# Kernel tuning notes

Measured on AMD Instinct MI355X. Metric: run time of the kernel, lower is better.

## Reference

```python
import jax, jax.numpy as jnp
import numpy as np

B, T, D_IN = 4, 512, 2048
H, G, HD = 16, 4, 128
CACHE = 3584
S = CACHE + T  # max_seq after cache concat
MAX_POS = 8192
EPS = 1e-6


def _rope_tables():
    inv_freq = 1.0 / (10000.0 ** (np.arange(0, HD, 2, dtype=np.float32) / HD))
    pos = np.arange(MAX_POS, dtype=np.float32)
    freqs = np.outer(pos, inv_freq)                      # [MAX_POS, HD//2]
    emb = np.concatenate([freqs, freqs], axis=-1)        # [MAX_POS, HD]
    return jnp.asarray(np.cos(emb)), jnp.asarray(np.sin(emb))


def setup_inputs() -> dict:
    key = jax.random.key(0)
    ks = jax.random.split(key, 8)
    cos, sin = _rope_tables()
    sc = 1.0 / float(np.sqrt(D_IN))
    x = jax.random.normal(ks[0], (B, T, D_IN), jnp.float32)
    mask = jnp.zeros((B, 1, T, S), bool)  # True = masked out
    position_ids = jnp.broadcast_to(CACHE + jnp.arange(T, dtype=jnp.int32), (B, T))
    cache_k = jax.random.normal(ks[1], (B, G, CACHE, HD), jnp.float32)
    cache_v = jax.random.normal(ks[2], (B, G, CACHE, HD), jnp.float32)
    q_w = jax.random.normal(ks[3], (D_IN, H * HD), jnp.float32) * sc
    k_w = jax.random.normal(ks[4], (D_IN, G * HD), jnp.float32) * sc
    v_w = jax.random.normal(ks[5], (D_IN, G * HD), jnp.float32) * sc
    o_w = jax.random.normal(ks[6], (H * HD, D_IN), jnp.float32) * sc
    qn_w = jnp.ones((HD,), jnp.float32)
    kn_w = jnp.ones((HD,), jnp.float32)
    return dict(x=x, mask=mask, cos=cos, sin=sin, position_ids=position_ids,
                cache_k=cache_k, cache_v=cache_v, q_w=q_w, k_w=k_w, v_w=v_w,
                o_w=o_w, qn_w=qn_w, kn_w=kn_w)


def _rms(z, w):
    return z * jax.lax.rsqrt(jnp.mean(z * z, axis=-1, keepdims=True) + EPS) * w


def _rot_half(z):
    z1, z2 = jnp.split(z, 2, axis=-1)
    return jnp.concatenate([-z2, z1], axis=-1)


def _rope(z, c, s):
    return z * c + _rot_half(z) * s


def reference(x, mask, cos, sin, position_ids, cache_k, cache_v,
              q_w, k_w, v_w, o_w, qn_w, kn_w):
    b, t, _ = x.shape
    # projections + per-head RMSNorm (norm over head_dim, order-independent of transpose)
    q = _rms((x @ q_w).reshape(b, t, H, HD), qn_w).transpose(0, 2, 1, 3)  # [b,H,t,hd]
    k = _rms((x @ k_w).reshape(b, t, G, HD), kn_w).transpose(0, 2, 1, 3)  # [b,G,t,hd]
    v = (x @ v_w).reshape(b, t, G, HD).transpose(0, 2, 1, 3)              # [b,G,t,hd]
    c = cos[position_ids][:, None]  # [b,1,t,hd]
    s = sin[position_ids][:, None]
    q = _rope(q, c, s)
    k = _rope(k, c, s)
    # KV-cache concat (uniform prev length == padded max_seq in the original)
    k_full = jnp.concatenate([cache_k, k], axis=2)  # [b,G,S,hd]
    v_full = jnp.concatenate([cache_v, v], axis=2)
    # GQA attention: group queries over KV heads
    qg = q.reshape(b, G, H // G, t, HD)
    scores = jnp.einsum('bghtd,bgsd->bghts', qg, k_full) * (1.0 / float(np.sqrt(HD)))
    scores = scores + jnp.where(mask[:, :, None], -jnp.inf, 0.0)  # mask [b,1,t,S]->[b,1,1,t,S]
    attn = jax.nn.softmax(scores, axis=-1)
    ctx = jnp.einsum('bghts,bgsd->bghtd', attn, v_full)
    ctx = ctx.reshape(b, H, t, HD).transpose(0, 2, 1, 3).reshape(b, t, H * HD)
    return (ctx @ o_w, k_full, v_full)
```

## Files before the change

kernel.cpp:

```cpp
#include <hip/hip_runtime.h>
#include <stdint.h>

typedef unsigned short u16;
typedef __attribute__((ext_vector_type(4))) float f32x4;
typedef __attribute__((ext_vector_type(8))) short s16x8;

__device__ inline u16 f2b(float f){
    uint32_t u = __builtin_bit_cast(uint32_t, f);
    uint32_t r = (u + 0x7fffu + ((u >> 16) & 1u)) >> 16;
    return (u16)r;
}
__device__ inline float b2f(u16 u){
    uint32_t x = ((uint32_t)u) << 16;
    return __builtin_bit_cast(float, x);
}

__global__ void convert_x_k(const float* __restrict__ src, u16* __restrict__ dst, int n4){
    int i = blockIdx.x * blockDim.x + threadIdx.x;
    if (i >= n4) return;
    float4 v = ((const float4*)src)[i];
    ushort4 o; o.x = f2b(v.x); o.y = f2b(v.y); o.z = f2b(v.z); o.w = f2b(v.w);
    ((ushort4*)dst)[i] = o;
}

__global__ void transpose_convert_k(const float* __restrict__ src, u16* __restrict__ dst,
                                    int srcCols, int dstLd, int rowOff){
    __shared__ float ls[64][68];
    int r0 = blockIdx.x * 64;
    int c0 = blockIdx.y * 64;
    int t = threadIdx.x;
    #pragma unroll
    for (int i = 0; i < 4; i++){
        int r = i * 16 + (t >> 4);
        int c = (t & 15) * 4;
        float4 v = *(const float4*)(src + (size_t)(r0 + r) * srcCols + c0 + c);
        *(float4*)&ls[r][c] = v;
    }
    __syncthreads();
    #pragma unroll
    for (int i = 0; i < 2; i++){
        int rr = i * 32 + (t >> 3);
        int cc = (t & 7) * 8;
        union { u16 u[8]; uint4 v; } o;
        #pragma unroll
        for (int j = 0; j < 8; j++) o.u[j] = f2b(ls[cc + j][rr]);
        *(uint4*)(dst + (size_t)(rowOff + c0 + rr) * dstLd + r0 + cc) = o.v;
    }
}

__global__ void copy_cache_k_k(const float* __restrict__ ck, float* __restrict__ kfull,
                               u16* __restrict__ kbf, int n4){
    int i = blockIdx.x * blockDim.x + threadIdx.x;
    if (i >= n4) return;
    const int per_bg = 3584 * 128 / 4;
    int bg = i / per_bg, rem = i - bg * per_bg;
    float4 v = ((const float4*)ck)[i];
    size_t dst4 = (size_t)bg * (4096 * 128 / 4) + rem;
    ((float4*)kfull)[dst4] = v;
    ushort4 o; o.x = f2b(v.x); o.y = f2b(v.y); o.z = f2b(v.z); o.w = f2b(v.w);
    ((ushort4*)kbf)[dst4] = o;
}

__global__ void transpose_cache_v_k(const float* __restrict__ cv, float* __restrict__ vfull,
                                    u16* __restrict__ vT){
    __shared__ float ls[64][68];
    int bg = blockIdx.z;
    int s0 = blockIdx.x * 64;
    int d0 = blockIdx.y * 64;
    int t = threadIdx.x;
    #pragma unroll
    for (int i = 0; i < 4; i++){
        int r = i * 16 + (t >> 4);
        int c = (t & 15) * 4;
        float4 v = *(const float4*)(cv + ((size_t)bg * 3584 + s0 + r) * 128 + d0 + c);
        *(float4*)&ls[r][c] = v;
        *(float4*)(vfull + ((size_t)bg * 4096 + s0 + r) * 128 + d0 + c) = v;
    }
    __syncthreads();
    #pragma unroll
    for (int i = 0; i < 2; i++){
        int rr = i * 32 + (t >> 3);
        int cc = (t & 7) * 8;
        union { u16 u[8]; uint4 v; } o;
        #pragma unroll
        for (int j = 0; j < 8; j++) o.u[j] = f2b(ls[cc + j][rr]);
        *(uint4*)(vT + ((size_t)bg * 128 + d0 + rr) * 4096 + s0 + cc) = o.v;
    }
}

__global__ __launch_bounds__(256) void gemm_bt_k(const u16* __restrict__ A, const u16* __restrict__ Bt,
                                                 float* __restrict__ C, int K, int N){
    __shared__ u16 As[128][72];
    __shared__ u16 Bs[128][72];
    int m0 = blockIdx.y * 128;
    int n0 = blockIdx.x * 128;
    int t = threadIdx.x;
    int wave = t >> 6, lane = t & 63;
    int g16 = lane >> 4, l16 = lane & 15;
    int wr = (wave >> 1) * 64, wc = (wave & 1) * 64;
    f32x4 acc[4][4] = {};
    for (int k0 = 0; k0 < K; k0 += 64){
        #pragma unroll
        for (int i = 0; i < 4; i++){
            int r = i * 32 + (t >> 3);
            int cg = (t & 7) * 8;
            *(uint4*)&As[r][cg] = *(const uint4*)(A + (size_t)(m0 + r) * K + k0 + cg);
            *(uint4*)&Bs[r][cg] = *(const uint4*)(Bt + (size_t)(n0 + r) * K + k0 + cg);
        }
        __syncthreads();
        #pragma unroll
        for (int kc = 0; kc < 2; kc++){
            s16x8 af[4], bfx[4];
            #pragma unroll
            for (int mi = 0; mi < 4; mi++) af[mi]  = *(const s16x8*)&As[wr + mi * 16 + l16][kc * 32 + g16 * 8];
            #pragma unroll
            for (int ni = 0; ni < 4; ni++) bfx[ni] = *(const s16x8*)&Bs[wc + ni * 16 + l16][kc * 32 + g16 * 8];
            #pragma unroll
            for (int mi = 0; mi < 4; mi++)
                #pragma unroll
                for (int ni = 0; ni < 4; ni++)
                    acc[mi][ni] = __builtin_amdgcn_mfma_f32_16x16x32_bf16(af[mi], bfx[ni], acc[mi][ni], 0, 0, 0);
        }
        __syncthreads();
    }
    #pragma unroll
    for (int mi = 0; mi < 4; mi++)
        #pragma unroll
        for (int ni = 0; ni < 4; ni++)
            #pragma unroll
            for (int r = 0; r < 4; r++){
                int row = m0 + wr + mi * 16 + g16 * 4 + r;
                int col = n0 + wc + ni * 16 + l16;
                C[(size_t)row * N + col] = acc[mi][ni][r];
            }
}

__global__ void norm_rope_k(const float* __restrict__ proj, const int* __restrict__ pos_ids,
                            const float* __restrict__ cosT, const float* __restrict__ sinT,
                            const float* __restrict__ qn, const float* __restrict__ kn,
                            u16* __restrict__ qbf, u16* __restrict__ kbf, u16* __restrict__ vT,
                            float* __restrict__ kfull, float* __restrict__ vfull){
    int row = blockIdx.x;
    int b = row >> 9, tt = row & 511;
    int wave = threadIdx.x >> 6, lane = threadIdx.x & 63;
    int pos = pos_ids[row];
    float c0 = cosT[(size_t)pos * 128 + lane];
    float c1 = cosT[(size_t)pos * 128 + 64 + lane];
    float s0 = sinT[(size_t)pos * 128 + lane];
    float s1 = sinT[(size_t)pos * 128 + 64 + lane];
    for (int hh = wave * 6; hh < wave * 6 + 6; hh++){
        const float* z = proj + (size_t)row * 3072 + hh * 128;
        float z0 = z[lane], z1 = z[64 + lane];
        if (hh < 20){
            float ss = z0 * z0 + z1 * z1;
            #pragma unroll
            for (int m = 1; m < 64; m <<= 1) ss += __shfl_xor(ss, m);
            float rn = rsqrtf(ss * (1.0f / 128.0f) + 1e-6f);
            const float* w = (hh < 16) ? qn : kn;
            float zn0 = z0 * rn * w[lane], zn1 = z1 * rn * w[64 + lane];
            float o0 = zn0 * c0 - zn1 * s0;
            float o1 = zn1 * c1 + zn0 * s1;
            if (hh < 16){
                u16* q = qbf + (((size_t)(b * 16 + hh)) * 512 + tt) * 128;
                q[lane] = f2b(o0); q[64 + lane] = f2b(o1);
            } else {
                int g = hh - 16;
                size_t idx = (((size_t)(b * 4 + g)) * 4096 + 3584 + tt) * 128;
                kfull[idx + lane] = o0; kfull[idx + 64 + lane] = o1;
                kbf[idx + lane] = f2b(o0); kbf[idx + 64 + lane] = f2b(o1);
            }
        } else {
            int g = hh - 20;
            size_t idx = (((size_t)(b * 4 + g)) * 4096 + 3584 + tt) * 128;
            vfull[idx + lane] = z0; vfull[idx + 64 + lane] = z1;
            size_t tb = ((size_t)(b * 4 + g)) * 128;
            vT[(tb + lane) * 4096 + 3584 + tt] = f2b(z0);
            vT[(tb + 64 + lane) * 4096 + 3584 + tt] = f2b(z1);
        }
    }
}

__global__ __launch_bounds__(256) void attn_k(const u16* __restrict__ qbf, const u16* __restrict__ kbf,
                                              const u16* __restrict__ vT, u16* __restrict__ ctx){
    __shared__ u16 Ks[64][136];
    __shared__ u16 Vs[128][72];
    __shared__ u16 Ps[4][16][72];
    int qblk = blockIdx.x;
    int h = blockIdx.y;
    int b = blockIdx.z;
    int g = h >> 2;
    int t = threadIdx.x, wave = t >> 6, lane = t & 63;
    int g16 = lane >> 4, l16 = lane & 15;
    int q0 = qblk * 64 + wave * 16;
    const u16* qrow = qbf + (((size_t)(b * 16 + h)) * 512 + q0 + l16) * 128;
    s16x8 qf[4];
    #pragma unroll
    for (int kc = 0; kc < 4; kc++) qf[kc] = *(const s16x8*)(qrow + kc * 32 + g16 * 8);
    const u16* kbase = kbf + ((size_t)(b * 4 + g)) * 4096 * 128;
    const u16* vbase = vT + ((size_t)(b * 4 + g)) * 128 * 4096;
    float m[4], l[4];
    f32x4 acc[8] = {};
    #pragma unroll
    for (int r = 0; r < 4; r++){ m[r] = -1e30f; l[r] = 0.f; }
    const float scale = 0.08838834764831845f;

    for (int s0 = 0; s0 < 4096; s0 += 64){
        #pragma unroll
        for (int i = 0; i < 4; i++){
            int r = i * 16 + (t >> 4), cg = (t & 15) * 8;
            *(uint4*)&Ks[r][cg] = *(const uint4*)(kbase + (size_t)(s0 + r) * 128 + cg);
        }
        #pragma unroll
        for (int i = 0; i < 4; i++){
            int r = i * 32 + (t >> 3), cg = (t & 7) * 8;
            *(uint4*)&Vs[r][cg] = *(const uint4*)(vbase + (size_t)r * 4096 + s0 + cg);
        }
        __syncthreads();
        f32x4 sf[4] = {};
        #pragma unroll
        for (int ni = 0; ni < 4; ni++)
            #pragma unroll
            for (int kc = 0; kc < 4; kc++){
                s16x8 kfr = *(const s16x8*)&Ks[ni * 16 + l16][kc * 32 + g16 * 8];
                sf[ni] = __builtin_amdgcn_mfma_f32_16x16x32_bf16(qf[kc], kfr, sf[ni], 0, 0, 0);
            }
        float mn[4], esc[4];
        #pragma unroll
        for (int r = 0; r < 4; r++){
            float tmax = fmaxf(fmaxf(sf[0][r], sf[1][r]), fmaxf(sf[2][r], sf[3][r])) * scale;
            #pragma unroll
            for (int msk = 1; msk < 16; msk <<= 1) tmax = fmaxf(tmax, __shfl_xor(tmax, msk));
            mn[r] = fmaxf(m[r], tmax);
            esc[r] = __expf(m[r] - mn[r]);
        }
        float lsum[4] = {0.f, 0.f, 0.f, 0.f};
        #pragma unroll
        for (int ni = 0; ni < 4; ni++)
            #pragma unroll
            for (int r = 0; r < 4; r++){
                float p = __expf(sf[ni][r] * scale - mn[r]);
                lsum[r] += p;
                Ps[wave][g16 * 4 + r][ni * 16 + l16] = f2b(p);
            }
        #pragma unroll
        for (int r = 0; r < 4; r++){
            float ls = lsum[r];
            #pragma unroll
            for (int msk = 1; msk < 16; msk <<= 1) ls += __shfl_xor(ls, msk);
            l[r] = l[r] * esc[r] + ls;
            m[r] = mn[r];
        }
        #pragma unroll
        for (int dt = 0; dt < 8; dt++)
            #pragma unroll
            for (int r = 0; r < 4; r++) acc[dt][r] *= esc[r];
        asm volatile("s_waitcnt lgkmcnt(0)" ::: "memory");
        #pragma unroll
        for (int sc = 0; sc < 2; sc++){
            s16x8 pf = *(const s16x8*)&Ps[wave][l16][sc * 32 + g16 * 8];
            #pragma unroll
            for (int dt = 0; dt < 8; dt++){
                s16x8 vf = *(const s16x8*)&Vs[dt * 16 + l16][sc * 32 + g16 * 8];
                acc[dt] = __builtin_amdgcn_mfma_f32_16x16x32_bf16(pf, vf, acc[dt], 0, 0, 0);
            }
        }
        __syncthreads();
    }
    #pragma unroll
    for (int r = 0; r < 4; r++){
        float inv = 1.0f / l[r];
        int qq = q0 + g16 * 4 + r;
        #pragma unroll
        for (int dt = 0; dt < 8; dt++){
            size_t off = ((size_t)b * 512 + qq) * 2048 + h * 128 + dt * 16 + l16;
            ctx[off] = f2b(acc[dt][r] * inv);
        }
    }
}

extern "C" void kernel_launch(void* const* d_in, const int* in_sizes, int n_in,
                              void* d_out, int out_size, void* d_ws, size_t ws_size,
                              hipStream_t stream){
    const float* x       = (const float*)d_in[0];
    const float* cosT    = (const float*)d_in[2];
    const float* sinT    = (const float*)d_in[3];
    const int*   pos     = (const int*)  d_in[4];
    const float* cache_k = (const float*)d_in[5];
    const float* cache_v = (const float*)d_in[6];
    const float* q_w     = (const float*)d_in[7];
    const float* k_w     = (const float*)d_in[8];
    const float* v_w     = (const float*)d_in[9];
    const float* o_w     = (const float*)d_in[10];
    const float* qn      = (const float*)d_in[11];
    const float* kn      = (const float*)d_in[12];

    float* out   = (float*)d_out;
    float* kfull = out + 4194304;
    float* vfull = out + 12582912;

    char* ws = (char*)d_ws;
    u16*  x_bf   = (u16*) (ws);
    u16*  wqkv_t = (u16*) (ws + 8388608);
    u16*  wo_t   = (u16*) (ws + 20971520);
    float* proj  = (float*)(ws + 29360128);
    u16*  q_bf   = (u16*) (ws + 54525952);
    u16*  k_bf   = (u16*) (ws + 62914560);
    u16*  vT_bf  = (u16*) (ws + 79691776);
    u16*  ctx_bf = (u16*) (ws + 96468992);

    convert_x_k<<<4096, 256, 0, stream>>>(x, x_bf, 1048576);
    transpose_convert_k<<<dim3(32, 32), 256, 0, stream>>>(q_w, wqkv_t, 2048, 2048, 0);
    transpose_convert_k<<<dim3(32,  8), 256, 0, stream>>>(k_w, wqkv_t,  512, 2048, 2048);
    transpose_convert_k<<<dim3(32,  8), 256, 0, stream>>>(v_w, wqkv_t,  512, 2048, 2560);
    transpose_convert_k<<<dim3(32, 32), 256, 0, stream>>>(o_w, wo_t,   2048, 2048, 0);
    copy_cache_k_k<<<7168, 256, 0, stream>>>(cache_k, kfull, k_bf, 1835008);
    transpose_cache_v_k<<<dim3(56, 2, 16), 256, 0, stream>>>(cache_v, vfull, vT_bf);
    gemm_bt_k<<<dim3(24, 16), 256, 0, stream>>>(x_bf, wqkv_t, proj, 2048, 3072);
    norm_rope_k<<<2048, 256, 0, stream>>>(proj, pos, cosT, sinT, qn, kn, q_bf, k_bf, vT_bf, kfull, vfull);
    attn_k<<<dim3(8, 16, 4), 256, 0, stream>>>(q_bf, k_bf, vT_bf, ctx_bf);
    gemm_bt_k<<<dim3(16, 16), 256, 0, stream>>>(ctx_bf, wo_t, out, 2048, 2048);
}
```

Before: 509.8 us.

## Rewrite attention as split-KV flash kernel with 32x32 MFMA and merge pass

Replaces the attention kernel with a split-KV version: each block handles 128 queries over half of the 4096 keys, using 32x32x16 bf16 MFMAs, double-buffered swizzled LDS with register-staged prefetch, exp2-based softmax with lazy rescaling, and permlane swaps to keep P in registers instead of going through LDS. A new merge kernel combines the two partial outputs using the saved max/sum stats. This aims to raise MFMA efficiency, overlap global loads with compute, and cut LDS traffic. In exchange it adds a bf16 partial buffer that is written and read again in the merge kernel, plus one extra launch; that buffer reuses the projection workspace region.

New measurement: 486.3 us. -4.6%, faster.

```diff
diff --git a/kernel.cpp b/kernel.cpp
--- a/kernel.cpp
+++ b/kernel.cpp
@@ -3,7 +3,9 @@
 
 typedef unsigned short u16;
 typedef __attribute__((ext_vector_type(4))) float f32x4;
+typedef __attribute__((ext_vector_type(16))) float f32x16;
 typedef __attribute__((ext_vector_type(8))) short s16x8;
+typedef __attribute__((ext_vector_type(2))) unsigned u32x2;
 
 __device__ inline u16 f2b(float f){
     uint32_t u = __builtin_bit_cast(uint32_t, f);
@@ -13,6 +15,14 @@
 __device__ inline float b2f(u16 u){
     uint32_t x = ((uint32_t)u) << 16;
     return __builtin_bit_cast(float, x);
+}
+__device__ inline u32x2 pswap(unsigned a, unsigned b){
+    return __builtin_amdgcn_permlane32_swap(a, b, false, false);
+}
+__device__ inline unsigned pkbf(float lo, float hi){
+    unsigned r;
+    asm("v_cvt_pk_bf16_f32 %0, %1, %2" : "=v"(r) : "v"(lo), "v"(hi));
+    return r;
 }
 
 __global__ void convert_x_k(const float* __restrict__ src, u16* __restrict__ dst, int n4){
@@ -180,102 +190,160 @@
     }
 }
 
-__global__ __launch_bounds__(256) void attn_k(const u16* __restrict__ qbf, const u16* __restrict__ kbf,
-                                              const u16* __restrict__ vT, u16* __restrict__ ctx){
-    __shared__ u16 Ks[64][136];
-    __shared__ u16 Vs[128][72];
-    __shared__ u16 Ps[4][16][72];
-    int qblk = blockIdx.x;
-    int h = blockIdx.y;
-    int b = blockIdx.z;
-    int g = h >> 2;
-    int t = threadIdx.x, wave = t >> 6, lane = t & 63;
-    int g16 = lane >> 4, l16 = lane & 15;
-    int q0 = qblk * 64 + wave * 16;
-    const u16* qrow = qbf + (((size_t)(b * 16 + h)) * 512 + q0 + l16) * 128;
-    s16x8 qf[4];
-    #pragma unroll
-    for (int kc = 0; kc < 4; kc++) qf[kc] = *(const s16x8*)(qrow + kc * 32 + g16 * 8);
-    const u16* kbase = kbf + ((size_t)(b * 4 + g)) * 4096 * 128;
-    const u16* vbase = vT + ((size_t)(b * 4 + g)) * 128 * 4096;
-    float m[4], l[4];
-    f32x4 acc[8] = {};
-    #pragma unroll
-    for (int r = 0; r < 4; r++){ m[r] = -1e30f; l[r] = 0.f; }
-    const float scale = 0.08838834764831845f;
-
-    for (int s0 = 0; s0 < 4096; s0 += 64){
-        #pragma unroll
-        for (int i = 0; i < 4; i++){
-            int r = i * 16 + (t >> 4), cg = (t & 15) * 8;
-            *(uint4*)&Ks[r][cg] = *(const uint4*)(kbase + (size_t)(s0 + r) * 128 + cg);
-        }
-        #pragma unroll
-        for (int i = 0; i < 4; i++){
-            int r = i * 32 + (t >> 3), cg = (t & 7) * 8;
-            *(uint4*)&Vs[r][cg] = *(const uint4*)(vbase + (size_t)r * 4096 + s0 + cg);
+__device__ inline void stage_load(uint4* kst, uint4* vst, const u16* kb, const u16* vb, int s0, int t){
+    #pragma unroll
+    for (int j = 0; j < 4; j++){
+        int i = t + 256 * j;
+        int kg = i >> 4, cg = i & 15;
+        kst[j] = *(const uint4*)(kb + (size_t)(s0 + kg) * 128 + cg * 8);
+    }
+    #pragma unroll
+    for (int j = 0; j < 4; j++){
+        int i = t + 256 * j;
+        int d = i >> 3, cg = i & 7;
+        vst[j] = *(const uint4*)(vb + (size_t)d * 4096 + s0 + cg * 8);
+    }
+}
+__device__ inline void stage_write(uint4* smb, const uint4* kst, const uint4* vst, int t){
+    #pragma unroll
+    for (int j = 0; j < 4; j++){
+        int i = t + 256 * j;
+        int kg = i >> 4, cg = i & 15;
+        smb[cg * 64 + (kg ^ (4 * (cg & 7)))] = kst[j];
+    }
+    #pragma unroll
+    for (int j = 0; j < 4; j++){
+        int i = t + 256 * j;
+        int d = i >> 3, cg = i & 7;
+        smb[1024 + cg * 128 + d] = vst[j];
+    }
+}
+
+__global__ __launch_bounds__(256, 2) void attn2_k(const u16* __restrict__ qbf, const u16* __restrict__ kbf,
+                                                  const u16* __restrict__ vT, u16* __restrict__ opart,
+                                                  float* __restrict__ stats){
+    __shared__ uint4 sm[4096];
+    int fid = blockIdx.x;
+    int swz = (fid & 7) * 64 + (fid >> 3);
+    int bg = swz >> 5;  int b = bg >> 2, g = bg & 3;
+    int lo5 = swz & 31;
+    int hq = g * 4 + (lo5 >> 3);
+    int qb = (lo5 >> 1) & 3;
+    int sh = lo5 & 1;
+    int t = threadIdx.x, w = t >> 6, lane = t & 63;
+    int l31 = lane & 31, h = lane >> 5;
+    int qw = qb * 128 + w * 32 + l31;
+    size_t qoff = (((size_t)(b * 16 + hq)) * 512 + qw) * 128;
+    s16x8 qf[8];
+    #pragma unroll
+    for (int m = 0; m < 8; m++) qf[m] = *(const s16x8*)(qbf + qoff + m * 16 + h * 8);
+
+    const u16* kb = kbf + ((size_t)bg) * 4096 * 128 + (size_t)sh * 2048 * 128;
+    const u16* vb = vT  + ((size_t)bg) * 128 * 4096 + (size_t)sh * 2048;
+
+    f32x16 oacc[4] = {};
+    float m2 = -1e30f, l = 0.f;
+    const float scl2 = 0.08838834764831845f * 1.4426950408889634f;
+
+    uint4 kst[4], vst[4];
+    stage_load(kst, vst, kb, vb, 0, t);
+    stage_write(sm, kst, vst, t);
+    __syncthreads();
+
+    for (int it = 0; it < 32; ++it){
+        const uint4* B = sm + (it & 1) * 2048;
+        if (it + 1 < 32) stage_load(kst, vst, kb, vb, (it + 1) * 64, t);
+
+        f32x16 st[2] = {};
+        #pragma unroll
+        for (int kt = 0; kt < 2; kt++)
+            #pragma unroll
+            for (int m = 0; m < 8; m++){
+                int c = 2 * m + h;
+                s16x8 kf = *(const s16x8*)&B[c * 64 + ((kt * 32 + l31) ^ (4 * (c & 7)))];
+                st[kt] = __builtin_amdgcn_mfma_f32_32x32x16_bf16(kf, qf[m], st[kt], 0, 0, 0);
+            }
+        float p[2][16];
+        float mx = -1e30f;
+        #pragma unroll
+        for (int kt = 0; kt < 2; kt++)
+            #pragma unroll
+            for (int r = 0; r < 16; r++){ float v = st[kt][r] * scl2; p[kt][r] = v; mx = fmaxf(mx, v); }
+        {   u32x2 rr = pswap(__builtin_bit_cast(unsigned, mx), __builtin_bit_cast(unsigned, mx));
+            mx = fmaxf(mx, __builtin_bit_cast(float, h ? rr.x : rr.y)); }
+        if (__any(mx > m2 + 8.f)){
+            float mn = fmaxf(m2, mx);
+            float esc = exp2f(m2 - mn);
+            m2 = mn; l *= esc;
+            #pragma unroll
+            for (int d = 0; d < 4; d++)
+                #pragma unroll
+                for (int r = 0; r < 16; r++) oacc[d][r] *= esc;
+        }
+        float ls = 0.f;
+        #pragma unroll
+        for (int kt = 0; kt < 2; kt++)
+            #pragma unroll
+            for (int r = 0; r < 16; r++){ float pv = exp2f(p[kt][r] - m2); p[kt][r] = pv; ls += pv; }
+        {   u32x2 rr = pswap(__builtin_bit_cast(unsigned, ls), __builtin_bit_cast(unsigned, ls));
+            l += ls + __builtin_bit_cast(float, h ? rr.x : rr.y); }
+        #pragma unroll
+        for (int kc = 0; kc < 4; kc++){
+            int tt = kc >> 1, cc = kc & 1;
+            unsigned A0 = pkbf(p[tt][8 * cc + 0], p[tt][8 * cc + 1]);
+            unsigned A1 = pkbf(p[tt][8 * cc + 2], p[tt][8 * cc + 3]);
+            unsigned B0 = pkbf(p[tt][8 * cc + 4], p[tt][8 * cc + 5]);
+            unsigned B1 = pkbf(p[tt][8 * cc + 6], p[tt][8 * cc + 7]);
+            u32x2 w02 = pswap(A0, B0);
+            u32x2 w13 = pswap(A1, B1);
+            uint4 bw; bw.x = w02.x; bw.y = w13.x; bw.z = w02.y; bw.w = w13.y;
+            s16x8 pb = __builtin_bit_cast(s16x8, bw);
+            #pragma unroll
+            for (int dt = 0; dt < 4; dt++){
+                s16x8 vf = *(const s16x8*)&B[1024 + (2 * kc + h) * 128 + dt * 32 + l31];
+                oacc[dt] = __builtin_amdgcn_mfma_f32_32x32x16_bf16(vf, pb, oacc[dt], 0, 0, 0);
+            }
         }
         __syncthreads();
-        f32x4 sf[4] = {};
-        #pragma unroll
-        for (int ni = 0; ni < 4; ni++)
-            #pragma unroll
-            for (int kc = 0; kc < 4; kc++){
-                s16x8 kfr = *(const s16x8*)&Ks[ni * 16 + l16][kc * 32 + g16 * 8];
-                sf[ni] = __builtin_amdgcn_mfma_f32_16x16x32_bf16(qf[kc], kfr, sf[ni], 0, 0, 0);
-            }
-        float mn[4], esc[4];
-        #pragma unroll
-        for (int r = 0; r < 4; r++){
-            float tmax = fmaxf(fmaxf(sf[0][r], sf[1][r]), fmaxf(sf[2][r], sf[3][r])) * scale;
-            #pragma unroll
-            for (int msk = 1; msk < 16; msk <<= 1) tmax = fmaxf(tmax, __shfl_xor(tmax, msk));
-            mn[r] = fmaxf(m[r], tmax);
-            esc[r] = __expf(m[r] - mn[r]);
-        }
-        float lsum[4] = {0.f, 0.f, 0.f, 0.f};
-        #pragma unroll
-        for (int ni = 0; ni < 4; ni++)
-            #pragma unroll
-            for (int r = 0; r < 4; r++){
-                float p = __expf(sf[ni][r] * scale - mn[r]);
-                lsum[r] += p;
-                Ps[wave][g16 * 4 + r][ni * 16 + l16] = f2b(p);
-            }
-        #pragma unroll
-        for (int r = 0; r < 4; r++){
-            float ls = lsum[r];
-            #pragma unroll
-            for (int msk = 1; msk < 16; msk <<= 1) ls += __shfl_xor(ls, msk);
-            l[r] = l[r] * esc[r] + ls;
-            m[r] = mn[r];
-        }
-        #pragma unroll
-        for (int dt = 0; dt < 8; dt++)
-            #pragma unroll
-            for (int r = 0; r < 4; r++) acc[dt][r] *= esc[r];
-        asm volatile("s_waitcnt lgkmcnt(0)" ::: "memory");
-        #pragma unroll
-        for (int sc = 0; sc < 2; sc++){
-            s16x8 pf = *(const s16x8*)&Ps[wave][l16][sc * 32 + g16 * 8];
-            #pragma unroll
-            for (int dt = 0; dt < 8; dt++){
-                s16x8 vf = *(const s16x8*)&Vs[dt * 16 + l16][sc * 32 + g16 * 8];
-                acc[dt] = __builtin_amdgcn_mfma_f32_16x16x32_bf16(pf, vf, acc[dt], 0, 0, 0);
-            }
-        }
+        if (it + 1 < 32) stage_write(sm + ((it + 1) & 1) * 2048, kst, vst, t);
         __syncthreads();
     }
-    #pragma unroll
-    for (int r = 0; r < 4; r++){
-        float inv = 1.0f / l[r];
-        int qq = q0 + g16 * 4 + r;
-        #pragma unroll
-        for (int dt = 0; dt < 8; dt++){
-            size_t off = ((size_t)b * 512 + qq) * 2048 + h * 128 + dt * 16 + l16;
-            ctx[off] = f2b(acc[dt][r] * inv);
-        }
-    }
+    size_t rid = ((size_t)(b * 16 + hq)) * 512 + qw;
+    u16* ob = opart + ((size_t)sh * 32768 + rid) * 128;
+    #pragma unroll
+    for (int dt = 0; dt < 4; dt++)
+        #pragma unroll
+        for (int rg = 0; rg < 4; rg++){
+            ushort4 o4;
+            o4.x = f2b(oacc[dt][4 * rg + 0]); o4.y = f2b(oacc[dt][4 * rg + 1]);
+            o4.z = f2b(oacc[dt][4 * rg + 2]); o4.w = f2b(oacc[dt][4 * rg + 3]);
+            *(ushort4*)(ob + dt * 32 + 8 * rg + 4 * h) = o4;
+        }
+    if (h == 0){
+        float2 s2; s2.x = m2; s2.y = l;
+        *(float2*)(stats + ((size_t)sh * 32768 + rid) * 2) = s2;
+    }
+}
+
+__global__ void merge_k(const u16* __restrict__ opart, const float* __restrict__ stats,
+                        u16* __restrict__ ctx){
+    int gid = blockIdx.x * 256 + threadIdx.x;
+    int rid = gid >> 5, dg = (gid & 31) * 4;
+    float m0 = stats[(size_t)rid * 2], l0 = stats[(size_t)rid * 2 + 1];
+    float m1 = stats[65536 + (size_t)rid * 2], l1 = stats[65536 + (size_t)rid * 2 + 1];
+    float M = fmaxf(m0, m1);
+    float w0 = exp2f(m0 - M), w1 = exp2f(m1 - M);
+    float inv = 1.f / (l0 * w0 + l1 * w1);
+    ushort4 a = *(const ushort4*)(opart + (size_t)rid * 128 + dg);
+    ushort4 c4 = *(const ushort4*)(opart + 4194304ll + (size_t)rid * 128 + dg);
+    int b = rid >> 13, hq = (rid >> 9) & 15, q = rid & 511;
+    u16* dst = ctx + ((size_t)(b * 512 + q)) * 2048 + hq * 128 + dg;
+    ushort4 o;
+    o.x = f2b((b2f(a.x) * w0 + b2f(c4.x) * w1) * inv);
+    o.y = f2b((b2f(a.y) * w0 + b2f(c4.y) * w1) * inv);
+    o.z = f2b((b2f(a.z) * w0 + b2f(c4.z) * w1) * inv);
+    o.w = f2b((b2f(a.w) * w0 + b2f(c4.w) * w1) * inv);
+    *(ushort4*)dst = o;
 }
 
 extern "C" void kernel_launch(void* const* d_in, const int* in_sizes, int n_in,
@@ -303,6 +371,8 @@
     u16*  wqkv_t = (u16*) (ws + 8388608);
     u16*  wo_t   = (u16*) (ws + 20971520);
     float* proj  = (float*)(ws + 29360128);
+    u16*  opart  = (u16*) (ws + 29360128);
+    float* stats = (float*)(ws + 46137344);
     u16*  q_bf   = (u16*) (ws + 54525952);
     u16*  k_bf   = (u16*) (ws + 62914560);
     u16*  vT_bf  = (u16*) (ws + 79691776);
@@ -317,6 +387,7 @@
     transpose_cache_v_k<<<dim3(56, 2, 16), 256, 0, stream>>>(cache_v, vfull, vT_bf);
     gemm_bt_k<<<dim3(24, 16), 256, 0, stream>>>(x_bf, wqkv_t, proj, 2048, 3072);
     norm_rope_k<<<2048, 256, 0, stream>>>(proj, pos, cosT, sinT, qn, kn, q_bf, k_bf, vT_bf, kfull, vfull);
-    attn_k<<<dim3(8, 16, 4), 256, 0, stream>>>(q_bf, k_bf, vT_bf, ctx_bf);
+    attn2_k<<<512, 256, 0, stream>>>(q_bf, k_bf, vT_bf, opart, stats);
+    merge_k<<<4096, 256, 0, stream>>>(opart, stats, ctx_bf);
     gemm_bt_k<<<dim3(16, 16), 256, 0, stream>>>(ctx_bf, wo_t, out, 2048, 2048);
 }
```
